# Optimization experiments

Hardware: AMD Instinct MI355X
Metric: run time of the kernel (lower is better)

Reference implementation:

```python
import jax, jax.numpy as jnp
import numpy as np

N, F, B = 16384, 1024, 512


def setup_inputs() -> dict:
    key = jax.random.key(0)
    k1, k2, k3, k4, k5 = jax.random.split(key, 5)
    s = 1.0 / np.sqrt(F + B)
    return {
        "behavior": jax.random.normal(k1, (N, B), dtype=jnp.float32),
        "h_prev": jax.random.normal(k2, (N, F), dtype=jnp.float32),
        "c_prev": jax.random.normal(k3, (N, F), dtype=jnp.float32),
        "Wh": jax.random.normal(k4, (4 * F, F), dtype=jnp.float32) * s,
        "Wx": jax.random.normal(k5, (4 * F, B), dtype=jnp.float32) * s,
        "b": jnp.zeros((4 * F,), dtype=jnp.float32),
    }


def reference(behavior, h_prev, c_prev, Wh, Wx, b):
    # Fused single GEMM for all 4 gates: [n, 4F]
    gates = jnp.einsum("nf,gf->ng", h_prev, Wh) + jnp.einsum("nb,gb->ng", behavior, Wx) + b
    i, f, g, o = jnp.split(gates, 4, axis=-1)
    i = jax.nn.sigmoid(i)
    f = jax.nn.sigmoid(f)
    g = jnp.tanh(g)
    o = jax.nn.sigmoid(o)
    c = f * c_prev + i * g
    h = o * jnp.tanh(c)
    return h
```

## Files before the change

kernel.cpp:

```cpp
#include <hip/hip_runtime.h>
#include <hip/hip_bf16.h>
#include <stdint.h>
#include <type_traits>

#define N_ROWS 16384
#define F_DIM  1024
#define B_DIM  512
#define K_DIM  1536
#define G_DIM  4096
#define NT     24
#define CB_STR 68

typedef __bf16 v8bf __attribute__((ext_vector_type(8)));
typedef float  v4f  __attribute__((ext_vector_type(4)));

typedef const void __attribute__((address_space(1)))* gptr1;
typedef void       __attribute__((address_space(3)))* lptr3;

__device__ __forceinline__ unsigned short f2bf(float x) {
    union { float f; unsigned int u; } c; c.f = x;
    unsigned int u = c.u;
    return (unsigned short)((u + 0x7FFFu + ((u >> 16) & 1u)) >> 16);
}

__device__ __forceinline__ float sigmoidf_fast(float x) {
    return 1.f / (1.f + __expf(-x));
}
__device__ __forceinline__ float tanhf_fast(float x) {
    return 1.f - 2.f / (__expf(2.f * x) + 1.f);
}

__global__ void pack_all(const float* __restrict__ behavior,
                         const float* __restrict__ h_prev,
                         const float* __restrict__ Wh,
                         const float* __restrict__ Wx,
                         const float* __restrict__ b,
                         unsigned short* __restrict__ A,
                         unsigned short* __restrict__ W,
                         float* __restrict__ bperm) {
    const int blk = blockIdx.x;
    const int col = threadIdx.x * 8;
    const float* src;
    unsigned short* dst;
    if (blk < N_ROWS) {
        src = (col < F_DIM) ? h_prev + (long)blk * F_DIM + col
                            : behavior + (long)blk * B_DIM + (col - F_DIM);
        dst = A + (long)blk * K_DIM + col;
    } else {
        const int gp   = blk - N_ROWS;
        const int gate = gp & 3;
        const int f    = gp >> 2;
        const int g    = gate * F_DIM + f;
        src = (col < F_DIM) ? Wh + (long)g * F_DIM + col
                            : Wx + (long)g * B_DIM + (col - F_DIM);
        dst = W + (long)gp * K_DIM + col;
        if (threadIdx.x == 0) bperm[gp] = b[g];
    }
    float4 lo = *(const float4*)src;
    float4 hi = *(const float4*)(src + 4);
    union { unsigned short u[8]; int4 v; } p;
    p.u[0] = f2bf(lo.x); p.u[1] = f2bf(lo.y); p.u[2] = f2bf(lo.z); p.u[3] = f2bf(lo.w);
    p.u[4] = f2bf(hi.x); p.u[5] = f2bf(hi.y); p.u[6] = f2bf(hi.z); p.u[7] = f2bf(hi.w);
    *(int4*)dst = p.v;
}

__global__ __launch_bounds__(512, 2) void lstm_gemm(
    const unsigned short* __restrict__ A,
    const unsigned short* __restrict__ W,
    const float* __restrict__ bperm,
    const float* __restrict__ c_prev,
    float* __restrict__ out)
{
    extern __shared__ char smem[];

    const int bid = blockIdx.x;
    const int n0  = (bid & 15) << 8;
    const int m0  = (bid >> 4) << 8;

    const int tid  = threadIdx.x;
    const int lane = tid & 63;
    const int wave = tid >> 6;
    const int wmi  = wave >> 2;
    const int wni  = wave & 3;
    const int lrow = lane & 15;
    const int quad = lane >> 4;

    const int g7  = lrow & 7;
    const int cs0 = (quad ^ g7) << 4;
    const int cs1 = ((4 + quad) ^ g7) << 4;
    const int aRd = wmi * 16384 + lrow * 128;
    const int bRd = wni * 8192  + lrow * 128;

    const int srow = lane >> 3;
    const int schk = (lane & 7) ^ srow;
    const unsigned short* sA = A + (long)(m0 + wave * 8 + srow) * K_DIM + schk * 8;
    const unsigned short* sB = W + (long)(n0 + wave * 8 + srow) * K_DIM + schk * 8;
    const int sDst = wave * 1024;

    v4f acc[8][4] = {};

    auto stage1 = [&](const unsigned short* src, int ldsbase, int u, int koff) {
        __builtin_amdgcn_global_load_lds(
            (gptr1)(src + (long)u * 64 * K_DIM + koff),
            (lptr3)(smem + ldsbase + u * 8192 + sDst), 16, 0, 0);
    };

    auto tile = [&](int BUF, int kn, auto pf_tag) {
        constexpr bool PF = decltype(pf_tag)::value;
        const int Ab = BUF * 32768;
        const int Bb = 65536 + Ab;
        const int Pb = (BUF ^ 1) * 32768;
        v8bf afr[2][2], bfr[4][2];

        if constexpr (PF) {
#pragma unroll
            for (int u = 0; u < 4; ++u) stage1(sB, 65536 + Pb, u, kn);
#pragma unroll
            for (int u = 0; u < 4; ++u) stage1(sA, Pb, u, kn);
        }

#pragma unroll
        for (int nt = 0; nt < 4; ++nt) {
            bfr[nt][0] = *(const v8bf*)(smem + Bb + bRd + nt * 2048 + cs0);
            bfr[nt][1] = *(const v8bf*)(smem + Bb + bRd + nt * 2048 + cs1);
        }

#pragma unroll
        for (int Q = 0; Q < 4; ++Q) {
            afr[0][0] = *(const v8bf*)(smem + Ab + aRd + (2*Q    ) * 2048 + cs0);
            afr[0][1] = *(const v8bf*)(smem + Ab + aRd + (2*Q    ) * 2048 + cs1);
            afr[1][0] = *(const v8bf*)(smem + Ab + aRd + (2*Q + 1) * 2048 + cs0);
            afr[1][1] = *(const v8bf*)(smem + Ab + aRd + (2*Q + 1) * 2048 + cs1);
            __builtin_amdgcn_s_setprio(1);
#pragma unroll
            for (int kh = 0; kh < 2; ++kh)
#pragma unroll
                for (int j = 0; j < 2; ++j)
#pragma unroll
                    for (int nt = 0; nt < 4; ++nt)
                        acc[2*Q + j][nt] = __builtin_amdgcn_mfma_f32_16x16x32_bf16(
                            afr[j][kh], bfr[nt][kh], acc[2*Q + j][nt], 0, 0, 0);
            __builtin_amdgcn_s_setprio(0);
        }

        asm volatile("s_waitcnt vmcnt(0)" ::: "memory");
        __builtin_amdgcn_s_barrier();
    };

#pragma unroll
    for (int u = 0; u < 4; ++u) stage1(sB, 65536, u, 0);
#pragma unroll
    for (int u = 0; u < 4; ++u) stage1(sA, 0, u, 0);
    asm volatile("s_waitcnt vmcnt(0)" ::: "memory");
    __builtin_amdgcn_s_barrier();

    int kn = 64;
    for (int t = 0; t < NT - 1; ++t) {
        tile(t & 1, kn, std::true_type{});
        kn += 64;
    }
    tile((NT - 1) & 1, 0, std::false_type{});

    float* cbuf = (float*)smem;
    const int fbase = n0 >> 2;
#pragma unroll
    for (int i = 0; i < 8; ++i) {
        const int q  = i * 512 + tid;
        const int r  = q >> 4;
        const int c4 = (q & 15) << 2;
        *(float4*)&cbuf[r * CB_STR + c4] =
            *(const float4*)&c_prev[(long)(m0 + r) * F_DIM + fbase + c4];
    }
    __syncthreads();

    const int l3 = lane & 3;
    const int fl = (lane >> 2) & 3;
#pragma unroll
    for (int nt = 0; nt < 4; ++nt) {
        const int   gcol = n0 + wni * 64 + nt * 16 + lrow;
        const float bias = bperm[gcol];
#pragma unroll
        for (int mt = 0; mt < 8; ++mt) {
            float a0 = acc[mt][nt][0] + bias;
            float a1 = acc[mt][nt][1] + bias;
            float a2 = acc[mt][nt][2] + bias;
            float a3 = acc[mt][nt][3] + bias;
            float s0 = (lane & 1) ? a0 : a1;
            float s1 = (lane & 1) ? a2 : a3;
            float t0 = __shfl_xor(s0, 1, 64);
            float t1 = __shfl_xor(s1, 1, 64);
            if (lane & 1) { a0 = t0; a2 = t1; } else { a1 = t0; a3 = t1; }
            s0 = (lane & 2) ? a0 : a2;
            s1 = (lane & 2) ? a1 : a3;
            t0 = __shfl_xor(s0, 2, 64);
            t1 = __shfl_xor(s1, 2, 64);
            if (lane & 2) { a0 = t0; a1 = t1; } else { a2 = t0; a3 = t1; }
            const float iv = sigmoidf_fast(a0);
            const float fv = sigmoidf_fast(a1);
            const float gv = tanhf_fast(a2);
            const float ov = sigmoidf_fast(a3);
            const int lr = wmi * 128 + mt * 16 + quad * 4 + l3;
            const int lc = wni * 16 + nt * 4 + fl;
            const float cp = cbuf[lr * CB_STR + lc];
            const float cv = fv * cp + iv * gv;
            cbuf[lr * CB_STR + lc] = ov * tanhf_fast(cv);
        }
    }
    __syncthreads();

#pragma unroll
    for (int i = 0; i < 8; ++i) {
        const int q  = i * 512 + tid;
        const int r  = q >> 4;
        const int c4 = (q & 15) << 2;
        *(float4*)&out[(long)(m0 + r) * F_DIM + fbase + c4] =
            *(const float4*)&cbuf[r * CB_STR + c4];
    }
}

extern "C" void kernel_launch(void* const* d_in, const int* in_sizes, int n_in,
                              void* d_out, int out_size, void* d_ws, size_t ws_size,
                              hipStream_t stream) {
    const float* behavior = (const float*)d_in[0];
    const float* h_prev   = (const float*)d_in[1];
    const float* c_prev   = (const float*)d_in[2];
    const float* Wh       = (const float*)d_in[3];
    const float* Wx       = (const float*)d_in[4];
    const float* b        = (const float*)d_in[5];
    float* out = (float*)d_out;

    unsigned short* A  = (unsigned short*)d_ws;
    unsigned short* W  = A + (size_t)N_ROWS * K_DIM;
    float*       bperm = (float*)(W + (size_t)G_DIM * K_DIM);

    hipFuncSetAttribute(reinterpret_cast<const void*>(lstm_gemm),
                        hipFuncAttributeMaxDynamicSharedMemorySize, 131072);

    pack_all<<<N_ROWS + G_DIM, 192, 0, stream>>>(behavior, h_prev, Wh, Wx, b, A, W, bperm);
    lstm_gemm<<<dim3((N_ROWS / 256) * (G_DIM / 256)), 512, 131072, stream>>>(A, W, bperm, c_prev, out);
}
```

Measured before the change: 423.2 us.

## Pre-swizzle operands into MFMA fragment layout and load directly from global

The pack kernel now writes A and W in a blocked layout that matches the MFMA 16x16x32 fragment order, so each lane's fragment is one contiguous 16-byte chunk. The GEMM drops LDS staging entirely and loads fragments straight from global memory into registers, with register double-buffering of the B fragments and A fragments loaded one step ahead. This removes LDS traffic, barriers and the async copy, and shrinks shared memory to the epilogue buffer. In exchange it relies on L2/L1 for reuse across waves, since each wave reloads the same data from global memory without sharing through LDS, so load latency may not be fully hidden.

```diff
diff --git a/kernel.cpp b/kernel.cpp
--- a/kernel.cpp
+++ b/kernel.cpp
@@ -1,7 +1,6 @@
 #include <hip/hip_runtime.h>
 #include <hip/hip_bf16.h>
 #include <stdint.h>
-#include <type_traits>
 
 #define N_ROWS 16384
 #define F_DIM  1024
@@ -14,9 +13,6 @@
 typedef __bf16 v8bf __attribute__((ext_vector_type(8)));
 typedef float  v4f  __attribute__((ext_vector_type(4)));
 
-typedef const void __attribute__((address_space(1)))* gptr1;
-typedef void       __attribute__((address_space(3)))* lptr3;
-
 __device__ __forceinline__ unsigned short f2bf(float x) {
     union { float f; unsigned int u; } c; c.f = x;
     unsigned int u = c.u;
@@ -35,25 +31,28 @@
                          const float* __restrict__ Wh,
                          const float* __restrict__ Wx,
                          const float* __restrict__ b,
-                         unsigned short* __restrict__ A,
-                         unsigned short* __restrict__ W,
+                         unsigned short* __restrict__ A2,
+                         unsigned short* __restrict__ W2,
                          float* __restrict__ bperm) {
     const int blk = blockIdx.x;
     const int col = threadIdx.x * 8;
     const float* src;
-    unsigned short* dst;
+    unsigned short* dstbase;
+    int row;
     if (blk < N_ROWS) {
-        src = (col < F_DIM) ? h_prev + (long)blk * F_DIM + col
-                            : behavior + (long)blk * B_DIM + (col - F_DIM);
-        dst = A + (long)blk * K_DIM + col;
+        row = blk;
+        src = (col < F_DIM) ? h_prev + (long)row * F_DIM + col
+                            : behavior + (long)row * B_DIM + (col - F_DIM);
+        dstbase = A2;
     } else {
         const int gp   = blk - N_ROWS;
         const int gate = gp & 3;
         const int f    = gp >> 2;
         const int g    = gate * F_DIM + f;
+        row = gp;
         src = (col < F_DIM) ? Wh + (long)g * F_DIM + col
                             : Wx + (long)g * B_DIM + (col - F_DIM);
-        dst = W + (long)gp * K_DIM + col;
+        dstbase = W2;
         if (threadIdx.x == 0) bperm[gp] = b[g];
     }
     float4 lo = *(const float4*)src;
@@ -61,12 +60,15 @@
     union { unsigned short u[8]; int4 v; } p;
     p.u[0] = f2bf(lo.x); p.u[1] = f2bf(lo.y); p.u[2] = f2bf(lo.z); p.u[3] = f2bf(lo.w);
     p.u[4] = f2bf(hi.x); p.u[5] = f2bf(hi.y); p.u[6] = f2bf(hi.z); p.u[7] = f2bf(hi.w);
-    *(int4*)dst = p.v;
+    const int kc   = col >> 5;
+    const int quad = (col >> 3) & 3;
+    const long off = ((long)(row >> 4) * 48 + kc) * 512 + (quad * 16 + (row & 15)) * 8;
+    *(int4*)(dstbase + off) = p.v;
 }
 
 __global__ __launch_bounds__(512, 2) void lstm_gemm(
-    const unsigned short* __restrict__ A,
-    const unsigned short* __restrict__ W,
+    const unsigned short* __restrict__ A2,
+    const unsigned short* __restrict__ W2,
     const float* __restrict__ bperm,
     const float* __restrict__ c_prev,
     float* __restrict__ out)
@@ -85,81 +87,64 @@
     const int lrow = lane & 15;
     const int quad = lane >> 4;
 
-    const int g7  = lrow & 7;
-    const int cs0 = (quad ^ g7) << 4;
-    const int cs1 = ((4 + quad) ^ g7) << 4;
-    const int aRd = wmi * 16384 + lrow * 128;
-    const int bRd = wni * 8192  + lrow * 128;
-
-    const int srow = lane >> 3;
-    const int schk = (lane & 7) ^ srow;
-    const unsigned short* sA = A + (long)(m0 + wave * 8 + srow) * K_DIM + schk * 8;
-    const unsigned short* sB = W + (long)(n0 + wave * 8 + srow) * K_DIM + schk * 8;
-    const int sDst = wave * 1024;
+    const unsigned short* pA = A2 + ((long)((m0 >> 4) + wmi * 8) * 48) * 512 + lane * 8;
+    const unsigned short* pB = W2 + ((long)((n0 >> 4) + wni * 4) * 48) * 512 + lane * 8;
 
     v4f acc[8][4] = {};
-
-    auto stage1 = [&](const unsigned short* src, int ldsbase, int u, int koff) {
-        __builtin_amdgcn_global_load_lds(
-            (gptr1)(src + (long)u * 64 * K_DIM + koff),
-            (lptr3)(smem + ldsbase + u * 8192 + sDst), 16, 0, 0);
-    };
-
-    auto tile = [&](int BUF, int kn, auto pf_tag) {
-        constexpr bool PF = decltype(pf_tag)::value;
-        const int Ab = BUF * 32768;
-        const int Bb = 65536 + Ab;
-        const int Pb = (BUF ^ 1) * 32768;
-        v8bf afr[2][2], bfr[4][2];
-
-        if constexpr (PF) {
-#pragma unroll
-            for (int u = 0; u < 4; ++u) stage1(sB, 65536 + Pb, u, kn);
-#pragma unroll
-            for (int u = 0; u < 4; ++u) stage1(sA, Pb, u, kn);
-        }
-
-#pragma unroll
-        for (int nt = 0; nt < 4; ++nt) {
-            bfr[nt][0] = *(const v8bf*)(smem + Bb + bRd + nt * 2048 + cs0);
-            bfr[nt][1] = *(const v8bf*)(smem + Bb + bRd + nt * 2048 + cs1);
-        }
-
-#pragma unroll
-        for (int Q = 0; Q < 4; ++Q) {
-            afr[0][0] = *(const v8bf*)(smem + Ab + aRd + (2*Q    ) * 2048 + cs0);
-            afr[0][1] = *(const v8bf*)(smem + Ab + aRd + (2*Q    ) * 2048 + cs1);
-            afr[1][0] = *(const v8bf*)(smem + Ab + aRd + (2*Q + 1) * 2048 + cs0);
-            afr[1][1] = *(const v8bf*)(smem + Ab + aRd + (2*Q + 1) * 2048 + cs1);
-            __builtin_amdgcn_s_setprio(1);
-#pragma unroll
-            for (int kh = 0; kh < 2; ++kh)
-#pragma unroll
-                for (int j = 0; j < 2; ++j)
-#pragma unroll
-                    for (int nt = 0; nt < 4; ++nt)
-                        acc[2*Q + j][nt] = __builtin_amdgcn_mfma_f32_16x16x32_bf16(
-                            afr[j][kh], bfr[nt][kh], acc[2*Q + j][nt], 0, 0, 0);
-            __builtin_amdgcn_s_setprio(0);
-        }
-
-        asm volatile("s_waitcnt vmcnt(0)" ::: "memory");
-        __builtin_amdgcn_s_barrier();
-    };
-
-#pragma unroll
-    for (int u = 0; u < 4; ++u) stage1(sB, 65536, u, 0);
-#pragma unroll
-    for (int u = 0; u < 4; ++u) stage1(sA, 0, u, 0);
-    asm volatile("s_waitcnt vmcnt(0)" ::: "memory");
-    __builtin_amdgcn_s_barrier();
-
-    int kn = 64;
-    for (int t = 0; t < NT - 1; ++t) {
-        tile(t & 1, kn, std::true_type{});
-        kn += 64;
-    }
-    tile((NT - 1) & 1, 0, std::false_type{});
+    v8bf bfA[4][2], bfB[4][2];
+    v8bf af0[4], af1[4];
+
+#define LDAQ(dst, kO, QQ)                                                       \
+    dst[0] = *(const v8bf*)(pA + (kO) + ((QQ)*2    ) * 24576      );            \
+    dst[1] = *(const v8bf*)(pA + (kO) + ((QQ)*2    ) * 24576 + 512);            \
+    dst[2] = *(const v8bf*)(pA + (kO) + ((QQ)*2 + 1) * 24576      );            \
+    dst[3] = *(const v8bf*)(pA + (kO) + ((QQ)*2 + 1) * 24576 + 512);
+
+#define LDBF(dst, kO, NT)                                                       \
+    dst[NT][0] = *(const v8bf*)(pB + (kO) + (NT) * 24576      );                \
+    dst[NT][1] = *(const v8bf*)(pB + (kO) + (NT) * 24576 + 512);
+
+#define MFMAQ(Q, AF, BF)                                                        \
+    __builtin_amdgcn_s_setprio(1);                                              \
+    _Pragma("unroll")                                                           \
+    for (int kh = 0; kh < 2; ++kh)                                              \
+        _Pragma("unroll")                                                       \
+        for (int j = 0; j < 2; ++j)                                             \
+            _Pragma("unroll")                                                   \
+            for (int nt = 0; nt < 4; ++nt)                                      \
+                acc[2*(Q)+j][nt] = __builtin_amdgcn_mfma_f32_16x16x32_bf16(     \
+                    AF[j*2+kh], BF[nt][kh], acc[2*(Q)+j][nt], 0, 0, 0);         \
+    __builtin_amdgcn_s_setprio(0);
+
+#define TILE(BC, BN, kO)                                                        \
+    LDAQ(af1, (kO), 1)                                            \
+    LDBF(BN, (kO) + 1024, 0)                                                    \
+    MFMAQ(0, af0, BC)                                                           \
+    LDAQ(af0, (kO), 2)                                            \
+    LDBF(BN, (kO) + 1024, 1)                                                    \
+    MFMAQ(1, af1, BC)                                                           \
+    LDAQ(af1, (kO), 3)                                            \
+    LDBF(BN, (kO) + 1024, 2)                                                    \
+    MFMAQ(2, af0, BC)                                                           \
+    LDAQ(af0, (kO) + 1024, 0)                               \
+    LDBF(BN, (kO) + 1024, 3)                                                    \
+    MFMAQ(3, af1, BC)
+
+    LDBF(bfA, 0, 0) LDBF(bfA, 0, 1) LDBF(bfA, 0, 2) LDBF(bfA, 0, 3)
+    LDAQ(af0, 0, 0)
+
+    int kO = 0;
+#pragma unroll 1
+    for (int p = 0; p < NT / 2; ++p) {
+        TILE(bfA, bfB, kO)
+        kO += 1024;
+        TILE(bfB, bfA, kO)
+        kO += 1024;
+    }
+#undef TILE
+#undef LDAQ
+#undef LDBF
+#undef MFMAQ
 
     float* cbuf = (float*)smem;
     const int fbase = n0 >> 2;
@@ -229,13 +214,13 @@
     const float* b        = (const float*)d_in[5];
     float* out = (float*)d_out;
 
-    unsigned short* A  = (unsigned short*)d_ws;
-    unsigned short* W  = A + (size_t)N_ROWS * K_DIM;
-    float*       bperm = (float*)(W + (size_t)G_DIM * K_DIM);
+    unsigned short* A2 = (unsigned short*)d_ws;
+    unsigned short* W2 = A2 + (size_t)N_ROWS * K_DIM;
+    float*       bperm = (float*)(W2 + (size_t)G_DIM * K_DIM);
 
     hipFuncSetAttribute(reinterpret_cast<const void*>(lstm_gemm),
-                        hipFuncAttributeMaxDynamicSharedMemorySize, 131072);
-
-    pack_all<<<N_ROWS + G_DIM, 192, 0, stream>>>(behavior, h_prev, Wh, Wx, b, A, W, bperm);
-    lstm_gemm<<<dim3((N_ROWS / 256) * (G_DIM / 256)), 512, 131072, stream>>>(A, W, bperm, c_prev, out);
-}
+                        hipFuncAttributeMaxDynamicSharedMemorySize, 69632);
+
+    pack_all<<<N_ROWS + G_DIM, 192, 0, stream>>>(behavior, h_prev, Wh, Wx, b, A2, W2, bperm);
+    lstm_gemm<<<dim3((N_ROWS / 256) * (G_DIM / 256)), 512, 69632, stream>>>(A2, W2, bperm, c_prev, out);
+}
```

After: 461.4 us. 9.0% more time.
